# Kernel optimization log

Measured on AMD Instinct MI355X. Metric: run time of the kernel, lower is better.

Reference implementation:

```python
import jax, jax.numpy as jnp
import numpy as np

B, H, L, D = 2, 16, 1024, 64
LMAX = 2048  # max_sequence_length: patterns built & normalized at LMAX, then sliced to L
PI = float(np.pi)


def _scale_pattern(freq):
    # pattern[h, t, d] = exp(i(t+ph)) + exp(i(2t+ph)) + exp(i(0.5t+ph)), ph = 2*pi*h/H
    # identical across d, so keep [H, L, 1] and broadcast over D
    phase = 2.0 * PI * jnp.arange(H, dtype=jnp.float32) / H          # [H]
    t = jnp.linspace(0.0, 2.0 * PI * freq, LMAX)                     # [LMAX]
    a1 = t[None, :] + phase[:, None]
    a2 = 2.0 * t[None, :] + phase[:, None]
    a3 = 0.5 * t[None, :] + phase[:, None]
    pr = jnp.cos(a1) + jnp.cos(a2) + jnp.cos(a3)                     # [H, LMAX]
    pi_ = jnp.sin(a1) + jnp.sin(a2) + jnp.sin(a3)
    norm = jnp.sqrt(jnp.sum(pr * pr + pi_ * pi_, axis=1, keepdims=True))  # over full LMAX
    pr, pi_ = pr / norm, pi_ / norm
    return pr[:, :L, None], pi_[:, :L, None]                          # [H, L, 1]


def _expert_total_pattern():
    # 8 experts x 3 aspects; pattern[t, d] = exp(i(f*t + 2*pi*d/D)), normalized per
    # column over LMAX (|exp|=1 -> norm sqrt(LMAX)). Elementwise complex multiply is
    # linear, so the expert stage equals x * sum(all patterns)/(sqrt(3)*sqrt(8)).
    freqs = np.array([[0.3 + 0.1 * i, 0.2 + 0.1 * i, 0.1 + 0.1 * i]
                      for i in range(8)], dtype=np.float32).reshape(-1)   # [24]
    t = jnp.linspace(0.0, 2.0 * PI, LMAX)                                 # [LMAX]
    phase_d = 2.0 * PI * jnp.arange(D, dtype=jnp.float32) / D             # [D]
    ang = jnp.asarray(freqs)[:, None, None] * t[None, :, None] + phase_d[None, None, :]  # [24, LMAX, D]
    col_norm = 1.0 / np.sqrt(float(LMAX))
    denom = np.sqrt(3.0) * np.sqrt(8.0)
    pr = jnp.sum(jnp.cos(ang), axis=0) * (col_norm / denom)               # [LMAX, D]
    pi_ = jnp.sum(jnp.sin(ang), axis=0) * (col_norm / denom)
    return pr[:L], pi_[:L]                                                # [L, D]


def _process_scale(Qr, Qi, Kr, Ki, Vr, Vi, pr, pi_):
    # complex elementwise pattern multiply
    Qpr = Qr * pr - Qi * pi_
    Qpi = Qr * pi_ + Qi * pr
    Kpr = Kr * pr - Ki * pi_
    Kpi = Kr * pi_ + Ki * pr
    # complex scores = Qp @ Kp^T (no conjugation, matching the torch code)
    sr = jnp.einsum('bhld,bhmd->bhlm', Qpr, Kpr) - jnp.einsum('bhld,bhmd->bhlm', Qpi, Kpi)
    si = jnp.einsum('bhld,bhmd->bhlm', Qpr, Kpi) + jnp.einsum('bhld,bhmd->bhlm', Qpi, Kpr)
    mag = jnp.sqrt(sr * sr + si * si) / np.sqrt(float(D))
    w = jax.nn.softmax(mag, axis=-1)
    return (jnp.einsum('bhlm,bhmd->bhld', w, Vr),
            jnp.einsum('bhlm,bhmd->bhld', w, Vi))


def reference(Q_real, Q_imag, K_real, K_imag, V_real, V_imag):
    scale_freqs = [1.0, 0.5, 0.25, 0.1]  # char, word, phrase, sentence
    acc_r = jnp.zeros_like(Q_real)
    acc_i = jnp.zeros_like(Q_real)
    for f in scale_freqs:
        pr, pi_ = _scale_pattern(f)
        o_r, o_i = _process_scale(Q_real, Q_imag, K_real, K_imag, V_real, V_imag, pr, pi_)
        acc_r = acc_r + o_r
        acc_i = acc_i + o_i
    inv = 1.0 / np.sqrt(float(len(scale_freqs)))
    acc_r = acc_r * inv
    acc_i = acc_i * inv
    # expert mixing (linear in x -> single fused complex elementwise multiply)
    epr, epi = _expert_total_pattern()  # [L, D], broadcast over B,H
    out_r = acc_r * epr - acc_i * epi
    out_i = acc_r * epi + acc_i * epr
    return jnp.stack([out_r, out_i], axis=0)  # [2, B, H, L, D] (real, imag)


def setup_inputs() -> dict:
    key = jax.random.key(0)
    ks = jax.random.split(key, 6)
    shape = (B, H, L, D)
    names = ['Q_real', 'Q_imag', 'K_real', 'K_imag', 'V_real', 'V_imag']
    return {n: jax.random.normal(k, shape, dtype=jnp.float32) for n, k in zip(names, ks)}
```

## Files before the change

kernel.cpp:

```cpp
#include <hip/hip_runtime.h>
#include <math.h>

typedef short bf16x8 __attribute__((ext_vector_type(8)));
typedef float f32x4 __attribute__((ext_vector_type(4)));

#define BDIM 256
constexpr int B_ = 2, H_ = 16, L_ = 1024, D_ = 64, LMAX_ = 2048;
constexpr int BH_ = B_ * H_;
constexpr float PI_F = 3.14159265358979323846f;

constexpr int WS_SVP = 0;
constexpr int WS_KBR = 65536;
constexpr int WS_KBI = WS_KBR + 1048576;
constexpr int WS_VTR = WS_KBI + 1048576;
constexpr int WS_VTI = WS_VTR + 1048576;

__device__ __forceinline__ unsigned short f2b(float x) {
    union { float f; unsigned u; } v; v.f = x;
    return (unsigned short)((v.u + 0x8000u) >> 16);
}
__device__ __forceinline__ unsigned pk2(float a, float b) {
    union { float f; unsigned u; } va, vb; va.f = a; vb.f = b;
    return ((va.u + 0x8000u) >> 16) | ((vb.u + 0x8000u) & 0xFFFF0000u);
}
__device__ __forceinline__ uint4 pack4(const float4& a, const float4& b) {
    return make_uint4(pk2(a.x, a.y), pk2(a.z, a.w), pk2(b.x, b.y), pk2(b.z, b.w));
}

#define MFMA(a, b, c) __builtin_amdgcn_mfma_f32_16x16x32_bf16((a), (b), (c), 0, 0, 0)

__device__ __forceinline__ float a_val(int s, int l, float4 invn) {
    const float fr = (s == 0) ? 1.0f : (s == 1) ? 0.5f : (s == 2) ? 0.25f : 0.1f;
    const float iv = (s == 0) ? invn.x : (s == 1) ? invn.y : (s == 2) ? invn.z : invn.w;
    float t = (2.0f * PI_F * fr / (float)(LMAX_ - 1)) * (float)l;
    float m2 = 3.0f + 2.0f * cosf(t) + 2.0f * cosf(0.5f * t) + 2.0f * cosf(1.5f * t);
    return sqrtf(fmaxf(m2, 0.0f)) * iv;
}

__global__ __launch_bounds__(BDIM)
void prep_kernel(const float* __restrict__ Kr, const float* __restrict__ Ki,
                 const float* __restrict__ Vr, const float* __restrict__ Vi,
                 float* __restrict__ ws) {
    const int tid = threadIdx.x;
    const int blk = blockIdx.x;
    unsigned short* KbR = (unsigned short*)(ws + WS_KBR);
    unsigned short* KbI = (unsigned short*)(ws + WS_KBI);
    unsigned short* VtR = (unsigned short*)(ws + WS_VTR);
    unsigned short* VtI = (unsigned short*)(ws + WS_VTI);

    if (blk < 256) {
        const int comp = blk >> 7;
        const float* src = comp ? Ki : Kr;
        unsigned short* dst = comp ? KbI : KbR;
        size_t b0 = (size_t)(blk & 127) * 16384;
#pragma unroll
        for (int i = 0; i < 4; ++i) {
            size_t e = b0 + (size_t)(i * 256 + tid) * 16;
            float4 x0 = *(const float4*)(src + e);
            float4 x1 = *(const float4*)(src + e + 4);
            float4 x2 = *(const float4*)(src + e + 8);
            float4 x3 = *(const float4*)(src + e + 12);
            *(uint4*)(dst + e) = pack4(x0, x1);
            *(uint4*)(dst + e + 8) = pack4(x2, x3);
        }
    } else {
        __shared__ unsigned short sT[64 * 70];
        __shared__ float sRed[4 * 64];
        const int vb = blk - 256;
        const int comp = vb & 1, mt = (vb >> 1) & 15, bh = vb >> 5;
        const int m0 = mt * 64;
        const float* src = (comp ? Vi : Vr) + (size_t)bh * 65536 + (size_t)m0 * 64;
        unsigned short* dstA = (comp ? VtI : VtR) + (size_t)bh * 65536;
#pragma unroll
        for (int i = 0; i < 4; ++i) {
            int e = i * 256 + tid;
            int m = e >> 4, d4 = (e & 15) * 4;
            float4 x = *(const float4*)(src + (size_t)m * 64 + d4);
            *(uint2*)&sT[m * 70 + d4] = make_uint2(pk2(x.x, x.y), pk2(x.z, x.w));
        }
        {
            int d = tid & 63, grp = tid >> 6;
            float s = 0.0f;
#pragma unroll
            for (int k = 0; k < 16; ++k) s += src[(size_t)(grp * 16 + k) * 64 + d];
            sRed[grp * 64 + d] = s;
        }
        __syncthreads();
        {
            int d = tid >> 2, ms = (tid & 3) * 16;
            unsigned short v[16];
#pragma unroll
            for (int k = 0; k < 16; ++k) v[k] = sT[(ms + k) * 70 + d];
            unsigned short* dst = dstA + (size_t)d * 1024 + m0 + ms;
            *(uint4*)dst = make_uint4((unsigned)v[0] | ((unsigned)v[1] << 16),
                                      (unsigned)v[2] | ((unsigned)v[3] << 16),
                                      (unsigned)v[4] | ((unsigned)v[5] << 16),
                                      (unsigned)v[6] | ((unsigned)v[7] << 16));
            *(uint4*)(dst + 8) = make_uint4((unsigned)v[8] | ((unsigned)v[9] << 16),
                                            (unsigned)v[10] | ((unsigned)v[11] << 16),
                                            (unsigned)v[12] | ((unsigned)v[13] << 16),
                                            (unsigned)v[14] | ((unsigned)v[15] << 16));
        }
        if (tid < 64)
            ws[WS_SVP + comp * 32768 + bh * 1024 + mt * 64 + tid] =
                sRed[tid] + sRed[64 + tid] + sRed[128 + tid] + sRed[192 + tid];
    }
}

__device__ __forceinline__ void stage64s(const unsigned short* g0, int stride,
                                         unsigned short* lds, int w, int lane) {
#pragma unroll
    for (int i = 0; i < 2; ++i) {
        int c = w * 2 + i;
        int lrow = c * 8 + (lane >> 3);
        int lg = (lane & 7) ^ (lrow & 7);
        const unsigned short* src = g0 + (size_t)lrow * stride + lg * 8;
        __builtin_amdgcn_global_load_lds(
            (const __attribute__((address_space(1))) void*)src,
            (__attribute__((address_space(3))) void*)(lds + c * 512), 16, 0, 0);
    }
}
__device__ __forceinline__ bf16x8 ldfrag(const unsigned short* b, int row, int g) {
    return *(const bf16x8*)&b[row * 64 + ((g ^ (row & 7)) << 3)];
}

__global__ __launch_bounds__(BDIM, 2)
void attn_kernel(const float* __restrict__ Qr, const float* __restrict__ Qi,
                 const float* __restrict__ ws, float* __restrict__ out, float4 invn) {
    __shared__ unsigned short sK0[2][4096], sK1[2][4096];
    __shared__ unsigned short sV0[4096], sV1[4096];
    __shared__ unsigned short sE[4096];
    __shared__ unsigned short sMg[4096];
    __shared__ unsigned short sAmb[4 * 1032];
    __shared__ float sDen[4 * 64];

    const int tid = threadIdx.x;
    const int lane = tid & 63;
    const int w = tid >> 6;
    const int lo16 = lane & 15;
    const int quad = lane >> 4;
    const int blk = blockIdx.x;
    const int bh = (blk & 7) * 4 + (blk >> 7);
    const int qt = (blk >> 3) & 15;
    const int l0 = qt * 64;
    const size_t base = (size_t)bh * (L_ * D_);

    const unsigned short* gKr = (const unsigned short*)(ws + WS_KBR) + (size_t)bh * 65536;
    const unsigned short* gKi = (const unsigned short*)(ws + WS_KBI) + (size_t)bh * 65536;
    const unsigned short* gVr = (const unsigned short*)(ws + WS_VTR) + (size_t)bh * 65536;
    const unsigned short* gVi = (const unsigned short*)(ws + WS_VTI) + (size_t)bh * 65536;

    stage64s(gKr, 64, sK0[0], w, lane);
    stage64s(gKi, 64, sK1[0], w, lane);

    for (int e = tid; e < 4096; e += BDIM) {
        int s = e >> 10, l = e & 1023;
        sAmb[s * 1032 + l] = f2b(a_val(s, l, invn) * 0.125f);
    }

    bf16x8 fQr0, fQr1, fQi0, fQi1, fnQi0, fnQi1;
    {
        const int ql = l0 + w * 16 + lo16;
        const float* qr = Qr + base + (size_t)ql * 64;
        const float* qi = Qi + base + (size_t)ql * 64;
        float4 a0 = *(const float4*)(qr + quad * 8);
        float4 a1 = *(const float4*)(qr + quad * 8 + 4);
        float4 b0 = *(const float4*)(qr + 32 + quad * 8);
        float4 b1 = *(const float4*)(qr + 32 + quad * 8 + 4);
        *(uint4*)&fQr0 = pack4(a0, a1);
        *(uint4*)&fQr1 = pack4(b0, b1);
        a0 = *(const float4*)(qi + quad * 8);
        a1 = *(const float4*)(qi + quad * 8 + 4);
        b0 = *(const float4*)(qi + 32 + quad * 8);
        b1 = *(const float4*)(qi + 32 + quad * 8 + 4);
        *(uint4*)&fQi0 = pack4(a0, a1);
        *(uint4*)&fQi1 = pack4(b0, b1);
        uint4 t0 = *(uint4*)&fQi0, t1 = *(uint4*)&fQi1;
        t0.x ^= 0x80008000u; t0.y ^= 0x80008000u; t0.z ^= 0x80008000u; t0.w ^= 0x80008000u;
        t1.x ^= 0x80008000u; t1.y ^= 0x80008000u; t1.z ^= 0x80008000u; t1.w ^= 0x80008000u;
        *(uint4*)&fnQi0 = t0; *(uint4*)&fnQi1 = t1;
    }

    bf16x8 uf1a = (bf16x8){0, 0, 0, 0, 0, 0, 0, 0};
    uf1a[0] = (short)f2b(a_val(quad, l0 + w * 16 + lo16, invn) * (1.0f / 1024.0f));

    f32x4 accM1 = (f32x4){0.f, 0.f, 0.f, 0.f};
    f32x4 aOutR[4], aOutI[4];
#pragma unroll
    for (int dt = 0; dt < 4; ++dt) {
        aOutR[dt] = (f32x4){0.f, 0.f, 0.f, 0.f};
        aOutI[dt] = (f32x4){0.f, 0.f, 0.f, 0.f};
    }

    __syncthreads();

    int cur = 0;
#pragma unroll 1
    for (int mt = 0; mt < 16; ++mt) {
        const int m0 = mt * 64;
        stage64s(gVr + m0, 1024, sV0, w, lane);
        stage64s(gVi + m0, 1024, sV1, w, lane);
        if (mt < 15) {
            stage64s(gKr + (size_t)(m0 + 64) * 64, 64, sK0[cur ^ 1], w, lane);
            stage64s(gKi + (size_t)(m0 + 64) * 64, 64, sK1[cur ^ 1], w, lane);
        }
        const unsigned short* cK0 = sK0[cur];
        const unsigned short* cK1 = sK1[cur];

#pragma unroll
        for (int ct = 0; ct < 4; ++ct) {
            const int mrow = ct * 16 + lo16;
            bf16x8 kr0 = ldfrag(cK0, mrow, quad), kr1 = ldfrag(cK0, mrow, quad + 4);
            bf16x8 ki0 = ldfrag(cK1, mrow, quad), ki1 = ldfrag(cK1, mrow, quad + 4);
            f32x4 aR = (f32x4){0.f, 0.f, 0.f, 0.f};
            f32x4 aI = (f32x4){0.f, 0.f, 0.f, 0.f};
            __builtin_amdgcn_s_setprio(1);
            aR = MFMA(kr0, fQr0, aR);  aR = MFMA(kr1, fQr1, aR);
            aR = MFMA(ki0, fnQi0, aR); aR = MFMA(ki1, fnQi1, aR);
            aI = MFMA(ki0, fQr0, aI);  aI = MFMA(ki1, fQr1, aI);
            aI = MFMA(kr0, fQi0, aI);  aI = MFMA(kr1, fQi1, aI);
            __builtin_amdgcn_s_setprio(0);
            float mg0 = sqrtf(fmaf(aR[0], aR[0], aI[0] * aI[0]));
            float mg1 = sqrtf(fmaf(aR[1], aR[1], aI[1] * aI[1]));
            float mg2 = sqrtf(fmaf(aR[2], aR[2], aI[2] * aI[2]));
            float mg3 = sqrtf(fmaf(aR[3], aR[3], aI[3] * aI[3]));
            bf16x8 bf1 = (bf16x8){0, 0, 0, 0, 0, 0, 0, 0};
            bf1[0] = (short)sAmb[quad * 1032 + m0 + ct * 16 + lo16];
            f32x4 z = (f32x4){0.f, 0.f, 0.f, 0.f};
            f32x4 a1 = MFMA(bf1, uf1a, z);
            float p0 = mg0 * a1[0], p1 = mg1 * a1[1];
            float p2 = mg2 * a1[2], p3 = mg3 * a1[3];
            int l = w * 16 + lo16;
            int gph = (ct * 2 + (quad >> 1)) ^ (l & 7);
            *(uint2*)&sE[l * 64 + gph * 8 + (quad & 1) * 4] =
                make_uint2(pk2(p0, p1), pk2(p2, p3));
            *(uint2*)&sMg[l * 64 + gph * 8 + (quad & 1) * 4] =
                make_uint2(pk2(mg0, mg1), pk2(mg2, mg3));
        }
        {
            bf16x8 mf0 = ldfrag(sMg, w * 16 + lo16, quad);
            bf16x8 mf1 = ldfrag(sMg, w * 16 + lo16, quad + 4);
            bf16x8 b0 = (bf16x8){0, 0, 0, 0, 0, 0, 0, 0};
            bf16x8 b1 = (bf16x8){0, 0, 0, 0, 0, 0, 0, 0};
            if (lo16 < 4) {
                b0 = *(const bf16x8*)&sAmb[lo16 * 1032 + m0 + quad * 8];
                b1 = *(const bf16x8*)&sAmb[lo16 * 1032 + m0 + 32 + quad * 8];
            }
            accM1 = MFMA(mf0, b0, accM1);
            accM1 = MFMA(mf1, b1, accM1);
        }
        if (mt < 15) {
            asm volatile("s_waitcnt vmcnt(4)" ::: "memory");
        } else {
            asm volatile("s_waitcnt vmcnt(0)" ::: "memory");
        }
        __builtin_amdgcn_s_barrier();
        {
            bf16x8 pa0 = ldfrag(sE, w * 16 + lo16, quad);
            bf16x8 pa1 = ldfrag(sE, w * 16 + lo16, quad + 4);
            __builtin_amdgcn_s_setprio(1);
#pragma unroll
            for (int dt = 0; dt < 4; ++dt) {
                int dr = dt * 16 + lo16;
                bf16x8 vr0 = ldfrag(sV0, dr, quad), vr1 = ldfrag(sV0, dr, quad + 4);
                bf16x8 vi0 = ldfrag(sV1, dr, quad), vi1 = ldfrag(sV1, dr, quad + 4);
                aOutR[dt] = MFMA(pa0, vr0, aOutR[dt]);
                aOutR[dt] = MFMA(pa1, vr1, aOutR[dt]);
                aOutI[dt] = MFMA(pa0, vi0, aOutI[dt]);
                aOutI[dt] = MFMA(pa1, vi1, aOutI[dt]);
            }
            __builtin_amdgcn_s_setprio(0);
        }
        asm volatile("s_waitcnt vmcnt(0)" ::: "memory");
        __builtin_amdgcn_s_barrier();
        cur ^= 1;
    }

    if (lo16 < 4) {
#pragma unroll
        for (int reg = 0; reg < 4; ++reg) {
            int r = w * 16 + quad * 4 + reg;
            float alv = a_val(lo16, l0 + r, invn);
            sDen[lo16 * 64 + r] = 1.0f / (1024.0f + alv * accM1[reg]);
        }
    }
    float cden[4];
#pragma unroll
    for (int reg = 0; reg < 4; ++reg) {
        int r = w * 16 + quad * 4 + reg;
        cden[reg] = sDen[r] + sDen[64 + r] + sDen[128 + r] + sDen[192 + r];
    }

    const float cE = rsqrtf(2048.0f) * rsqrtf(24.0f);
    float eRr[4], eRi[4];
#pragma unroll
    for (int reg = 0; reg < 4; ++reg) {
        int lrow = l0 + w * 16 + quad * 4 + reg;
        float tl = (2.0f * PI_F / (float)(LMAX_ - 1)) * (float)lrow;
        float s1, c1;
        __sincosf(0.1f * tl, &s1, &c1);
        const float W[10] = {1.f, 2.f, 3.f, 3.f, 3.f, 3.f, 3.f, 3.f, 2.f, 1.f};
        float cr = c1, ci = s1;
        float er = W[0] * cr, ei = W[0] * ci;
#pragma unroll
        for (int k = 1; k < 10; ++k) {
            float nr = cr * c1 - ci * s1;
            float ni = cr * s1 + ci * c1;
            cr = nr; ci = ni;
            er = fmaf(W[k], cr, er);
            ei = fmaf(W[k], ci, ei);
        }
        eRr[reg] = er * cE;
        eRi[reg] = ei * cE;
    }

    const size_t ooff = (size_t)BH_ * L_ * D_;
#pragma unroll
    for (int dt = 0; dt < 4; ++dt) {
        int d = dt * 16 + lo16;
        float svr = 0.0f, svi = 0.0f;
#pragma unroll
        for (int q = 0; q < 16; ++q) {
            svr += ws[WS_SVP + bh * 1024 + q * 64 + d];
            svi += ws[WS_SVP + 32768 + bh * 1024 + q * 64 + d];
        }
        float sp, cp;
        __sincosf((2.0f * PI_F / 64.0f) * (float)d, &sp, &cp);
#pragma unroll
        for (int reg = 0; reg < 4; ++reg) {
            int lrow = l0 + w * 16 + quad * 4 + reg;
            float numR = fmaf(cden[reg], svr, aOutR[dt][reg]) * 0.5f;
            float numI = fmaf(cden[reg], svi, aOutI[dt][reg]) * 0.5f;
            float epr = cp * eRr[reg] - sp * eRi[reg];
            float epi = sp * eRr[reg] + cp * eRi[reg];
            size_t o = base + (size_t)lrow * 64 + d;
            out[o] = numR * epr - numI * epi;
            out[o + ooff] = numR * epi + numI * epr;
        }
    }
}

extern "C" void kernel_launch(void* const* d_in, const int* in_sizes, int n_in,
                              void* d_out, int out_size, void* d_ws, size_t ws_size,
                              hipStream_t stream) {
    const float* Qr = (const float*)d_in[0];
    const float* Qi = (const float*)d_in[1];
    const float* Kr = (const float*)d_in[2];
    const float* Ki = (const float*)d_in[3];
    const float* Vr = (const float*)d_in[4];
    const float* Vi = (const float*)d_in[5];
    float* ws = (float*)d_ws;
    float* out = (float*)d_out;

    const double fr[4] = {1.0, 0.5, 0.25, 0.1};
    float inv[4];
    for (int s = 0; s < 4; ++s) {
        double a = 2.0 * 3.14159265358979323846 * fr[s] / (double)(LMAX_ - 1);
        double S = 3.0 * LMAX_;
        const double mul[3] = {1.0, 0.5, 1.5};
        for (int k = 0; k < 3; ++k) {
            double x = a * mul[k];
            S += 2.0 * (cos(x * 1023.5) * sin(x * 1024.0) / sin(x * 0.5));
        }
        inv[s] = (float)(1.0 / sqrt(S));
    }
    float4 invn = make_float4(inv[0], inv[1], inv[2], inv[3]);

    prep_kernel<<<1280, BDIM, 0, stream>>>(Kr, Ki, Vr, Vi, ws);
    attn_kernel<<<512, BDIM, 0, stream>>>(Qr, Qi, ws, out, invn);
}
```

Baseline: 152.2 us.

## Fuse prep and attention into one cooperative kernel with grid sync

Merges the K/V bf16 conversion and transpose prep kernel into the attention kernel, using a cooperative launch and a grid-wide sync between the two phases. Shared memory is a union so the prep scratch reuses the attention buffers. The per-row amplitude values are now read back from the LDS table instead of being recomputed with cosines. This removes one kernel launch and its gap, at the cost of a grid barrier and a fallback to two kernels if the cooperative launch fails.

New measurement: 287.7 us. 89.1% more time.

```diff
diff --git a/kernel.cpp b/kernel.cpp
--- a/kernel.cpp
+++ b/kernel.cpp
@@ -1,5 +1,8 @@
 #include <hip/hip_runtime.h>
+#include <hip/hip_cooperative_groups.h>
 #include <math.h>
+
+namespace cg = cooperative_groups;
 
 typedef short bf16x8 __attribute__((ext_vector_type(8)));
 typedef float f32x4 __attribute__((ext_vector_type(4)));
@@ -18,6 +21,10 @@
 __device__ __forceinline__ unsigned short f2b(float x) {
     union { float f; unsigned u; } v; v.f = x;
     return (unsigned short)((v.u + 0x8000u) >> 16);
+}
+__device__ __forceinline__ float b2f(unsigned short x) {
+    union { unsigned u; float f; } v; v.u = ((unsigned)x) << 16;
+    return v.f;
 }
 __device__ __forceinline__ unsigned pk2(float a, float b) {
     union { float f; unsigned u; } va, vb; va.f = a; vb.f = b;
@@ -37,75 +44,19 @@
     return sqrtf(fmaxf(m2, 0.0f)) * iv;
 }
 
-__global__ __launch_bounds__(BDIM)
-void prep_kernel(const float* __restrict__ Kr, const float* __restrict__ Ki,
-                 const float* __restrict__ Vr, const float* __restrict__ Vi,
-                 float* __restrict__ ws) {
-    const int tid = threadIdx.x;
-    const int blk = blockIdx.x;
-    unsigned short* KbR = (unsigned short*)(ws + WS_KBR);
-    unsigned short* KbI = (unsigned short*)(ws + WS_KBI);
-    unsigned short* VtR = (unsigned short*)(ws + WS_VTR);
-    unsigned short* VtI = (unsigned short*)(ws + WS_VTI);
-
-    if (blk < 256) {
-        const int comp = blk >> 7;
-        const float* src = comp ? Ki : Kr;
-        unsigned short* dst = comp ? KbI : KbR;
-        size_t b0 = (size_t)(blk & 127) * 16384;
-#pragma unroll
-        for (int i = 0; i < 4; ++i) {
-            size_t e = b0 + (size_t)(i * 256 + tid) * 16;
-            float4 x0 = *(const float4*)(src + e);
-            float4 x1 = *(const float4*)(src + e + 4);
-            float4 x2 = *(const float4*)(src + e + 8);
-            float4 x3 = *(const float4*)(src + e + 12);
-            *(uint4*)(dst + e) = pack4(x0, x1);
-            *(uint4*)(dst + e + 8) = pack4(x2, x3);
-        }
-    } else {
-        __shared__ unsigned short sT[64 * 70];
-        __shared__ float sRed[4 * 64];
-        const int vb = blk - 256;
-        const int comp = vb & 1, mt = (vb >> 1) & 15, bh = vb >> 5;
-        const int m0 = mt * 64;
-        const float* src = (comp ? Vi : Vr) + (size_t)bh * 65536 + (size_t)m0 * 64;
-        unsigned short* dstA = (comp ? VtI : VtR) + (size_t)bh * 65536;
-#pragma unroll
-        for (int i = 0; i < 4; ++i) {
-            int e = i * 256 + tid;
-            int m = e >> 4, d4 = (e & 15) * 4;
-            float4 x = *(const float4*)(src + (size_t)m * 64 + d4);
-            *(uint2*)&sT[m * 70 + d4] = make_uint2(pk2(x.x, x.y), pk2(x.z, x.w));
-        }
-        {
-            int d = tid & 63, grp = tid >> 6;
-            float s = 0.0f;
-#pragma unroll
-            for (int k = 0; k < 16; ++k) s += src[(size_t)(grp * 16 + k) * 64 + d];
-            sRed[grp * 64 + d] = s;
-        }
-        __syncthreads();
-        {
-            int d = tid >> 2, ms = (tid & 3) * 16;
-            unsigned short v[16];
-#pragma unroll
-            for (int k = 0; k < 16; ++k) v[k] = sT[(ms + k) * 70 + d];
-            unsigned short* dst = dstA + (size_t)d * 1024 + m0 + ms;
-            *(uint4*)dst = make_uint4((unsigned)v[0] | ((unsigned)v[1] << 16),
-                                      (unsigned)v[2] | ((unsigned)v[3] << 16),
-                                      (unsigned)v[4] | ((unsigned)v[5] << 16),
-                                      (unsigned)v[6] | ((unsigned)v[7] << 16));
-            *(uint4*)(dst + 8) = make_uint4((unsigned)v[8] | ((unsigned)v[9] << 16),
-                                            (unsigned)v[10] | ((unsigned)v[11] << 16),
-                                            (unsigned)v[12] | ((unsigned)v[13] << 16),
-                                            (unsigned)v[14] | ((unsigned)v[15] << 16));
-        }
-        if (tid < 64)
-            ws[WS_SVP + comp * 32768 + bh * 1024 + mt * 64 + tid] =
-                sRed[tid] + sRed[64 + tid] + sRed[128 + tid] + sRed[192 + tid];
-    }
-}
+union SMem {
+    struct {
+        unsigned short sK0[2][4096], sK1[2][4096];
+        unsigned short sV0[4096], sV1[4096];
+        unsigned short sE[4096], sMg[4096];
+        unsigned short sAmb[4 * 1032];
+        float sDen[4 * 64];
+    } a;
+    struct {
+        unsigned short sT[64 * 70];
+        float sRed[4 * 64];
+    } p;
+};
 
 __device__ __forceinline__ void stage64s(const unsigned short* g0, int stride,
                                          unsigned short* lds, int w, int lane) {
@@ -124,16 +75,59 @@
     return *(const bf16x8*)&b[row * 64 + ((g ^ (row & 7)) << 3)];
 }
 
-__global__ __launch_bounds__(BDIM, 2)
-void attn_kernel(const float* __restrict__ Qr, const float* __restrict__ Qi,
-                 const float* __restrict__ ws, float* __restrict__ out, float4 invn) {
-    __shared__ unsigned short sK0[2][4096], sK1[2][4096];
-    __shared__ unsigned short sV0[4096], sV1[4096];
-    __shared__ unsigned short sE[4096];
-    __shared__ unsigned short sMg[4096];
-    __shared__ unsigned short sAmb[4 * 1032];
-    __shared__ float sDen[4 * 64];
-
+__device__ __forceinline__ void vt_tile(int vb, const float* __restrict__ Vr,
+                                        const float* __restrict__ Vi,
+                                        float* __restrict__ ws, SMem& sm) {
+    const int tid = threadIdx.x;
+    const int comp = vb & 1, mt = (vb >> 1) & 15, bh = vb >> 5;
+    const int m0 = mt * 64;
+    unsigned short* VtR = (unsigned short*)(ws + WS_VTR);
+    unsigned short* VtI = (unsigned short*)(ws + WS_VTI);
+    const float* src = (comp ? Vi : Vr) + (size_t)bh * 65536 + (size_t)m0 * 64;
+    unsigned short* dstA = (comp ? VtI : VtR) + (size_t)bh * 65536;
+    __syncthreads();
+#pragma unroll
+    for (int i = 0; i < 4; ++i) {
+        int e = i * 256 + tid;
+        int m = e >> 4, d4 = (e & 15) * 4;
+        float4 x = *(const float4*)(src + (size_t)m * 64 + d4);
+        *(uint2*)&sm.p.sT[m * 70 + d4] = make_uint2(pk2(x.x, x.y), pk2(x.z, x.w));
+    }
+    {
+        int d = tid & 63, grp = tid >> 6;
+        float s = 0.0f;
+#pragma unroll
+        for (int k = 0; k < 16; ++k) s += src[(size_t)(grp * 16 + k) * 64 + d];
+        sm.p.sRed[grp * 64 + d] = s;
+    }
+    __syncthreads();
+    {
+        int d = tid >> 2, ms = (tid & 3) * 16;
+        unsigned short v[16];
+#pragma unroll
+        for (int k = 0; k < 16; ++k) v[k] = sm.p.sT[(ms + k) * 70 + d];
+        unsigned short* dst = dstA + (size_t)d * 1024 + m0 + ms;
+        *(uint4*)dst = make_uint4((unsigned)v[0] | ((unsigned)v[1] << 16),
+                                  (unsigned)v[2] | ((unsigned)v[3] << 16),
+                                  (unsigned)v[4] | ((unsigned)v[5] << 16),
+                                  (unsigned)v[6] | ((unsigned)v[7] << 16));
+        *(uint4*)(dst + 8) = make_uint4((unsigned)v[8] | ((unsigned)v[9] << 16),
+                                        (unsigned)v[10] | ((unsigned)v[11] << 16),
+                                        (unsigned)v[12] | ((unsigned)v[13] << 16),
+                                        (unsigned)v[14] | ((unsigned)v[15] << 16));
+    }
+    if (tid < 64)
+        ws[WS_SVP + comp * 32768 + bh * 1024 + mt * 64 + tid] =
+            sm.p.sRed[tid] + sm.p.sRed[64 + tid] + sm.p.sRed[128 + tid] +
+            sm.p.sRed[192 + tid];
+}
+
+__device__ __forceinline__ void attn_body(const float* __restrict__ Qr,
+                                          const float* __restrict__ Qi,
+                                          const float* __restrict__ ws,
+                                          float* __restrict__ out, float4 invn,
+                                          SMem& sm, bool fillAmb) {
+    auto& A = sm.a;
     const int tid = threadIdx.x;
     const int lane = tid & 63;
     const int w = tid >> 6;
@@ -150,12 +144,14 @@
     const unsigned short* gVr = (const unsigned short*)(ws + WS_VTR) + (size_t)bh * 65536;
     const unsigned short* gVi = (const unsigned short*)(ws + WS_VTI) + (size_t)bh * 65536;
 
-    stage64s(gKr, 64, sK0[0], w, lane);
-    stage64s(gKi, 64, sK1[0], w, lane);
-
-    for (int e = tid; e < 4096; e += BDIM) {
-        int s = e >> 10, l = e & 1023;
-        sAmb[s * 1032 + l] = f2b(a_val(s, l, invn) * 0.125f);
+    stage64s(gKr, 64, A.sK0[0], w, lane);
+    stage64s(gKi, 64, A.sK1[0], w, lane);
+
+    if (fillAmb) {
+        for (int e = tid; e < 4096; e += BDIM) {
+            int s = e >> 10, l = e & 1023;
+            A.sAmb[s * 1032 + l] = f2b(a_val(s, l, invn) * 0.125f);
+        }
     }
 
     bf16x8 fQr0, fQr1, fQi0, fQi1, fnQi0, fnQi1;
@@ -181,9 +177,6 @@
         *(uint4*)&fnQi0 = t0; *(uint4*)&fnQi1 = t1;
     }
 
-    bf16x8 uf1a = (bf16x8){0, 0, 0, 0, 0, 0, 0, 0};
-    uf1a[0] = (short)f2b(a_val(quad, l0 + w * 16 + lo16, invn) * (1.0f / 1024.0f));
-
     f32x4 accM1 = (f32x4){0.f, 0.f, 0.f, 0.f};
     f32x4 aOutR[4], aOutI[4];
 #pragma unroll
@@ -193,19 +186,23 @@
     }
 
     __syncthreads();
+
+    bf16x8 uf1a = (bf16x8){0, 0, 0, 0, 0, 0, 0, 0};
+    uf1a[0] = (short)f2b(b2f(A.sAmb[quad * 1032 + (l0 + w * 16 + lo16)]) *
+                         (1.0f / 128.0f));
 
     int cur = 0;
 #pragma unroll 1
     for (int mt = 0; mt < 16; ++mt) {
         const int m0 = mt * 64;
-        stage64s(gVr + m0, 1024, sV0, w, lane);
-        stage64s(gVi + m0, 1024, sV1, w, lane);
+        stage64s(gVr + m0, 1024, A.sV0, w, lane);
+        stage64s(gVi + m0, 1024, A.sV1, w, lane);
         if (mt < 15) {
-            stage64s(gKr + (size_t)(m0 + 64) * 64, 64, sK0[cur ^ 1], w, lane);
-            stage64s(gKi + (size_t)(m0 + 64) * 64, 64, sK1[cur ^ 1], w, lane);
-        }
-        const unsigned short* cK0 = sK0[cur];
-        const unsigned short* cK1 = sK1[cur];
+            stage64s(gKr + (size_t)(m0 + 64) * 64, 64, A.sK0[cur ^ 1], w, lane);
+            stage64s(gKi + (size_t)(m0 + 64) * 64, 64, A.sK1[cur ^ 1], w, lane);
+        }
+        const unsigned short* cK0 = A.sK0[cur];
+        const unsigned short* cK1 = A.sK1[cur];
 
 #pragma unroll
         for (int ct = 0; ct < 4; ++ct) {
@@ -225,26 +222,26 @@
             float mg2 = sqrtf(fmaf(aR[2], aR[2], aI[2] * aI[2]));
             float mg3 = sqrtf(fmaf(aR[3], aR[3], aI[3] * aI[3]));
             bf16x8 bf1 = (bf16x8){0, 0, 0, 0, 0, 0, 0, 0};
-            bf1[0] = (short)sAmb[quad * 1032 + m0 + ct * 16 + lo16];
+            bf1[0] = (short)A.sAmb[quad * 1032 + m0 + ct * 16 + lo16];
             f32x4 z = (f32x4){0.f, 0.f, 0.f, 0.f};
             f32x4 a1 = MFMA(bf1, uf1a, z);
             float p0 = mg0 * a1[0], p1 = mg1 * a1[1];
             float p2 = mg2 * a1[2], p3 = mg3 * a1[3];
             int l = w * 16 + lo16;
             int gph = (ct * 2 + (quad >> 1)) ^ (l & 7);
-            *(uint2*)&sE[l * 64 + gph * 8 + (quad & 1) * 4] =
+            *(uint2*)&A.sE[l * 64 + gph * 8 + (quad & 1) * 4] =
                 make_uint2(pk2(p0, p1), pk2(p2, p3));
-            *(uint2*)&sMg[l * 64 + gph * 8 + (quad & 1) * 4] =
+            *(uint2*)&A.sMg[l * 64 + gph * 8 + (quad & 1) * 4] =
                 make_uint2(pk2(mg0, mg1), pk2(mg2, mg3));
         }
         {
-            bf16x8 mf0 = ldfrag(sMg, w * 16 + lo16, quad);
-            bf16x8 mf1 = ldfrag(sMg, w * 16 + lo16, quad + 4);
+            bf16x8 mf0 = ldfrag(A.sMg, w * 16 + lo16, quad);
+            bf16x8 mf1 = ldfrag(A.sMg, w * 16 + lo16, quad + 4);
             bf16x8 b0 = (bf16x8){0, 0, 0, 0, 0, 0, 0, 0};
             bf16x8 b1 = (bf16x8){0, 0, 0, 0, 0, 0, 0, 0};
             if (lo16 < 4) {
-                b0 = *(const bf16x8*)&sAmb[lo16 * 1032 + m0 + quad * 8];
-                b1 = *(const bf16x8*)&sAmb[lo16 * 1032 + m0 + 32 + quad * 8];
+                b0 = *(const bf16x8*)&A.sAmb[lo16 * 1032 + m0 + quad * 8];
+                b1 = *(const bf16x8*)&A.sAmb[lo16 * 1032 + m0 + 32 + quad * 8];
             }
             accM1 = MFMA(mf0, b0, accM1);
             accM1 = MFMA(mf1, b1, accM1);
@@ -256,14 +253,14 @@
         }
         __builtin_amdgcn_s_barrier();
         {
-            bf16x8 pa0 = ldfrag(sE, w * 16 + lo16, quad);
-            bf16x8 pa1 = ldfrag(sE, w * 16 + lo16, quad + 4);
+            bf16x8 pa0 = ldfrag(A.sE, w * 16 + lo16, quad);
+            bf16x8 pa1 = ldfrag(A.sE, w * 16 + lo16, quad + 4);
             __builtin_amdgcn_s_setprio(1);
 #pragma unroll
             for (int dt = 0; dt < 4; ++dt) {
                 int dr = dt * 16 + lo16;
-                bf16x8 vr0 = ldfrag(sV0, dr, quad), vr1 = ldfrag(sV0, dr, quad + 4);
-                bf16x8 vi0 = ldfrag(sV1, dr, quad), vi1 = ldfrag(sV1, dr, quad + 4);
+                bf16x8 vr0 = ldfrag(A.sV0, dr, quad), vr1 = ldfrag(A.sV0, dr, quad + 4);
+                bf16x8 vi0 = ldfrag(A.sV1, dr, quad), vi1 = ldfrag(A.sV1, dr, quad + 4);
                 aOutR[dt] = MFMA(pa0, vr0, aOutR[dt]);
                 aOutR[dt] = MFMA(pa1, vr1, aOutR[dt]);
                 aOutI[dt] = MFMA(pa0, vi0, aOutI[dt]);
@@ -280,15 +277,15 @@
 #pragma unroll
         for (int reg = 0; reg < 4; ++reg) {
             int r = w * 16 + quad * 4 + reg;
-            float alv = a_val(lo16, l0 + r, invn);
-            sDen[lo16 * 64 + r] = 1.0f / (1024.0f + alv * accM1[reg]);
+            float alv = b2f(A.sAmb[lo16 * 1032 + (l0 + r)]) * 8.0f;
+            A.sDen[lo16 * 64 + r] = 1.0f / (1024.0f + alv * accM1[reg]);
         }
     }
     float cden[4];
 #pragma unroll
     for (int reg = 0; reg < 4; ++reg) {
         int r = w * 16 + quad * 4 + reg;
-        cden[reg] = sDen[r] + sDen[64 + r] + sDen[128 + r] + sDen[192 + r];
+        cden[reg] = A.sDen[r] + A.sDen[64 + r] + A.sDen[128 + r] + A.sDen[192 + r];
     }
 
     const float cE = rsqrtf(2048.0f) * rsqrtf(24.0f);
@@ -338,6 +335,82 @@
             out[o + ooff] = numR * epi + numI * epr;
         }
     }
+}
+
+__global__ __launch_bounds__(BDIM, 2)
+void fused_kernel(const float* __restrict__ Qr, const float* __restrict__ Qi,
+                  const float* __restrict__ Kr, const float* __restrict__ Ki,
+                  const float* __restrict__ Vr, const float* __restrict__ Vi,
+                  float* __restrict__ ws, float* __restrict__ out, float4 invn) {
+    __shared__ SMem sm;
+    const int tid = threadIdx.x;
+    const int blk = blockIdx.x;
+
+    {
+        unsigned short* KbR = (unsigned short*)(ws + WS_KBR);
+        unsigned short* KbI = (unsigned short*)(ws + WS_KBI);
+        const int comp = blk >> 8;
+        const float* src = comp ? Ki : Kr;
+        unsigned short* dst = comp ? KbI : KbR;
+        size_t b0 = (size_t)(blk & 255) * 8192;
+#pragma unroll
+        for (int i = 0; i < 2; ++i) {
+            size_t e = b0 + (size_t)(i * 256 + tid) * 16;
+            float4 x0 = *(const float4*)(src + e);
+            float4 x1 = *(const float4*)(src + e + 4);
+            float4 x2 = *(const float4*)(src + e + 8);
+            float4 x3 = *(const float4*)(src + e + 12);
+            *(uint4*)(dst + e) = pack4(x0, x1);
+            *(uint4*)(dst + e + 8) = pack4(x2, x3);
+        }
+    }
+    for (int e = tid; e < 4096; e += BDIM) {
+        int s = e >> 10, l = e & 1023;
+        sm.a.sAmb[s * 1032 + l] = f2b(a_val(s, l, invn) * 0.125f);
+    }
+    vt_tile(blk * 2, Vr, Vi, ws, sm);
+    vt_tile(blk * 2 + 1, Vr, Vi, ws, sm);
+
+    __threadfence();
+    cg::this_grid().sync();
+
+    attn_body(Qr, Qi, ws, out, invn, sm, false);
+}
+
+__global__ __launch_bounds__(BDIM)
+void prep_kernel(const float* __restrict__ Kr, const float* __restrict__ Ki,
+                 const float* __restrict__ Vr, const float* __restrict__ Vi,
+                 float* __restrict__ ws) {
+    __shared__ SMem sm;
+    const int tid = threadIdx.x;
+    const int blk = blockIdx.x;
+    if (blk < 256) {
+        unsigned short* KbR = (unsigned short*)(ws + WS_KBR);
+        unsigned short* KbI = (unsigned short*)(ws + WS_KBI);
+        const int comp = blk >> 7;
+        const float* src = comp ? Ki : Kr;
+        unsigned short* dst = comp ? KbI : KbR;
+        size_t b0 = (size_t)(blk & 127) * 16384;
+#pragma unroll
+        for (int i = 0; i < 4; ++i) {
+            size_t e = b0 + (size_t)(i * 256 + tid) * 16;
+            float4 x0 = *(const float4*)(src + e);
+            float4 x1 = *(const float4*)(src + e + 4);
+            float4 x2 = *(const float4*)(src + e + 8);
+            float4 x3 = *(const float4*)(src + e + 12);
+            *(uint4*)(dst + e) = pack4(x0, x1);
+            *(uint4*)(dst + e + 8) = pack4(x2, x3);
+        }
+    } else {
+        vt_tile(blk - 256, Vr, Vi, ws, sm);
+    }
+}
+
+__global__ __launch_bounds__(BDIM, 2)
+void attn_kernel(const float* __restrict__ Qr, const float* __restrict__ Qi,
+                 const float* __restrict__ ws, float* __restrict__ out, float4 invn) {
+    __shared__ SMem sm;
+    attn_body(Qr, Qi, ws, out, invn, sm, true);
 }
 
 extern "C" void kernel_launch(void* const* d_in, const int* in_sizes, int n_in,
@@ -366,6 +439,12 @@
     }
     float4 invn = make_float4(inv[0], inv[1], inv[2], inv[3]);
 
-    prep_kernel<<<1280, BDIM, 0, stream>>>(Kr, Ki, Vr, Vi, ws);
-    attn_kernel<<<512, BDIM, 0, stream>>>(Qr, Qi, ws, out, invn);
-}
+    void* args[] = {(void*)&Qr, (void*)&Qi, (void*)&Kr, (void*)&Ki,
+                    (void*)&Vr, (void*)&Vi, (void*)&ws, (void*)&out, (void*)&invn};
+    hipError_t err = hipLaunchCooperativeKernel(fused_kernel, dim3(512), dim3(BDIM),
+                                                args, 0, stream);
+    if (err != hipSuccess) {
+        prep_kernel<<<1280, BDIM, 0, stream>>>(Kr, Ki, Vr, Vi, ws);
+        attn_kernel<<<512, BDIM, 0, stream>>>(Qr, Qi, ws, out, invn);
+    }
+}
```

## Double-buffer V tiles, compute magnitude sums in registers, transpose SVP layout

Applied to the files above, without the earlier changes.

V tiles are now double-buffered alongside K and prefetched one iteration ahead, so each loop iteration needs one barrier instead of two. The per-row magnitude-weighted sums are accumulated in registers with FMAs and cross-lane shuffles, replacing the sMg LDS round trip and the extra MFMAs. The partial-sum workspace is stored transposed so the epilogue can read it with contiguous float4 loads. These changes cost more LDS for the second V buffer and extra per-lane FMA work, and the LDS padding on sAmb is dropped, which may bring back bank conflicts.

Result: slower. 155.4 us (+2.1%).

```diff
diff --git a/kernel.cpp b/kernel.cpp
--- a/kernel.cpp
+++ b/kernel.cpp
@@ -18,6 +18,18 @@
 __device__ __forceinline__ unsigned short f2b(float x) {
     union { float f; unsigned u; } v; v.f = x;
     return (unsigned short)((v.u + 0x8000u) >> 16);
+}
+__device__ __forceinline__ float b2f(unsigned short x) {
+    union { unsigned u; float f; } v; v.u = ((unsigned)x) << 16;
+    return v.f;
+}
+__device__ __forceinline__ float blo(unsigned u) {
+    union { unsigned u; float f; } v; v.u = u << 16;
+    return v.f;
+}
+__device__ __forceinline__ float bhi(unsigned u) {
+    union { unsigned u; float f; } v; v.u = u & 0xFFFF0000u;
+    return v.f;
 }
 __device__ __forceinline__ unsigned pk2(float a, float b) {
     union { float f; unsigned u; } va, vb; va.f = a; vb.f = b;
@@ -102,7 +114,7 @@
                                             (unsigned)v[14] | ((unsigned)v[15] << 16));
         }
         if (tid < 64)
-            ws[WS_SVP + comp * 32768 + bh * 1024 + mt * 64 + tid] =
+            ws[WS_SVP + comp * 32768 + bh * 1024 + tid * 16 + mt] =
                 sRed[tid] + sRed[64 + tid] + sRed[128 + tid] + sRed[192 + tid];
     }
 }
@@ -128,11 +140,9 @@
 void attn_kernel(const float* __restrict__ Qr, const float* __restrict__ Qi,
                  const float* __restrict__ ws, float* __restrict__ out, float4 invn) {
     __shared__ unsigned short sK0[2][4096], sK1[2][4096];
-    __shared__ unsigned short sV0[4096], sV1[4096];
+    __shared__ unsigned short sV0[2][4096], sV1[2][4096];
     __shared__ unsigned short sE[4096];
-    __shared__ unsigned short sMg[4096];
-    __shared__ unsigned short sAmb[4 * 1032];
-    __shared__ float sDen[4 * 64];
+    __shared__ unsigned short sAmb[4 * 1024];
 
     const int tid = threadIdx.x;
     const int lane = tid & 63;
@@ -152,10 +162,12 @@
 
     stage64s(gKr, 64, sK0[0], w, lane);
     stage64s(gKi, 64, sK1[0], w, lane);
+    stage64s(gVr, 1024, sV0[0], w, lane);
+    stage64s(gVi, 1024, sV1[0], w, lane);
 
     for (int e = tid; e < 4096; e += BDIM) {
         int s = e >> 10, l = e & 1023;
-        sAmb[s * 1032 + l] = f2b(a_val(s, l, invn) * 0.125f);
+        sAmb[s * 1024 + l] = f2b(a_val(s, l, invn) * 0.125f);
     }
 
     bf16x8 fQr0, fQr1, fQi0, fQi1, fnQi0, fnQi1;
@@ -181,10 +193,13 @@
         *(uint4*)&fnQi0 = t0; *(uint4*)&fnQi1 = t1;
     }
 
+    __syncthreads();
+
     bf16x8 uf1a = (bf16x8){0, 0, 0, 0, 0, 0, 0, 0};
-    uf1a[0] = (short)f2b(a_val(quad, l0 + w * 16 + lo16, invn) * (1.0f / 1024.0f));
-
-    f32x4 accM1 = (f32x4){0.f, 0.f, 0.f, 0.f};
+    uf1a[0] = (short)f2b(b2f(sAmb[quad * 1024 + (l0 + w * 16 + lo16)]) *
+                         (1.0f / 128.0f));
+
+    float macc[4] = {0.f, 0.f, 0.f, 0.f};
     f32x4 aOutR[4], aOutI[4];
 #pragma unroll
     for (int dt = 0; dt < 4; ++dt) {
@@ -192,17 +207,17 @@
         aOutI[dt] = (f32x4){0.f, 0.f, 0.f, 0.f};
     }
 
-    __syncthreads();
-
-    int cur = 0;
 #pragma unroll 1
     for (int mt = 0; mt < 16; ++mt) {
         const int m0 = mt * 64;
-        stage64s(gVr + m0, 1024, sV0, w, lane);
-        stage64s(gVi + m0, 1024, sV1, w, lane);
+        const int cur = mt & 1;
+        asm volatile("s_waitcnt vmcnt(0)" ::: "memory");
+        __builtin_amdgcn_s_barrier();
         if (mt < 15) {
             stage64s(gKr + (size_t)(m0 + 64) * 64, 64, sK0[cur ^ 1], w, lane);
             stage64s(gKi + (size_t)(m0 + 64) * 64, 64, sK1[cur ^ 1], w, lane);
+            stage64s(gVr + m0 + 64, 1024, sV0[cur ^ 1], w, lane);
+            stage64s(gVi + m0 + 64, 1024, sV1[cur ^ 1], w, lane);
         }
         const unsigned short* cK0 = sK0[cur];
         const unsigned short* cK1 = sK1[cur];
@@ -224,8 +239,16 @@
             float mg1 = sqrtf(fmaf(aR[1], aR[1], aI[1] * aI[1]));
             float mg2 = sqrtf(fmaf(aR[2], aR[2], aI[2] * aI[2]));
             float mg3 = sqrtf(fmaf(aR[3], aR[3], aI[3] * aI[3]));
+#pragma unroll
+            for (int s = 0; s < 4; ++s) {
+                uint2 av = *(const uint2*)&sAmb[s * 1024 + m0 + ct * 16 + quad * 4];
+                macc[s] = fmaf(mg0, blo(av.x),
+                          fmaf(mg1, bhi(av.x),
+                          fmaf(mg2, blo(av.y),
+                          fmaf(mg3, bhi(av.y), macc[s]))));
+            }
             bf16x8 bf1 = (bf16x8){0, 0, 0, 0, 0, 0, 0, 0};
-            bf1[0] = (short)sAmb[quad * 1032 + m0 + ct * 16 + lo16];
+            bf1[0] = (short)sAmb[quad * 1024 + m0 + ct * 16 + lo16];
             f32x4 z = (f32x4){0.f, 0.f, 0.f, 0.f};
             f32x4 a1 = MFMA(bf1, uf1a, z);
             float p0 = mg0 * a1[0], p1 = mg1 * a1[1];
@@ -234,27 +257,7 @@
             int gph = (ct * 2 + (quad >> 1)) ^ (l & 7);
             *(uint2*)&sE[l * 64 + gph * 8 + (quad & 1) * 4] =
                 make_uint2(pk2(p0, p1), pk2(p2, p3));
-            *(uint2*)&sMg[l * 64 + gph * 8 + (quad & 1) * 4] =
-                make_uint2(pk2(mg0, mg1), pk2(mg2, mg3));
-        }
-        {
-            bf16x8 mf0 = ldfrag(sMg, w * 16 + lo16, quad);
-            bf16x8 mf1 = ldfrag(sMg, w * 16 + lo16, quad + 4);
-            bf16x8 b0 = (bf16x8){0, 0, 0, 0, 0, 0, 0, 0};
-            bf16x8 b1 = (bf16x8){0, 0, 0, 0, 0, 0, 0, 0};
-            if (lo16 < 4) {
-                b0 = *(const bf16x8*)&sAmb[lo16 * 1032 + m0 + quad * 8];
-                b1 = *(const bf16x8*)&sAmb[lo16 * 1032 + m0 + 32 + quad * 8];
-            }
-            accM1 = MFMA(mf0, b0, accM1);
-            accM1 = MFMA(mf1, b1, accM1);
-        }
-        if (mt < 15) {
-            asm volatile("s_waitcnt vmcnt(4)" ::: "memory");
-        } else {
-            asm volatile("s_waitcnt vmcnt(0)" ::: "memory");
-        }
-        __builtin_amdgcn_s_barrier();
+        }
         {
             bf16x8 pa0 = ldfrag(sE, w * 16 + lo16, quad);
             bf16x8 pa1 = ldfrag(sE, w * 16 + lo16, quad + 4);
@@ -262,8 +265,8 @@
 #pragma unroll
             for (int dt = 0; dt < 4; ++dt) {
                 int dr = dt * 16 + lo16;
-                bf16x8 vr0 = ldfrag(sV0, dr, quad), vr1 = ldfrag(sV0, dr, quad + 4);
-                bf16x8 vi0 = ldfrag(sV1, dr, quad), vi1 = ldfrag(sV1, dr, quad + 4);
+                bf16x8 vr0 = ldfrag(sV0[cur], dr, quad), vr1 = ldfrag(sV0[cur], dr, quad + 4);
+                bf16x8 vi0 = ldfrag(sV1[cur], dr, quad), vi1 = ldfrag(sV1[cur], dr, quad + 4);
                 aOutR[dt] = MFMA(pa0, vr0, aOutR[dt]);
                 aOutR[dt] = MFMA(pa1, vr1, aOutR[dt]);
                 aOutI[dt] = MFMA(pa0, vi0, aOutI[dt]);
@@ -271,25 +274,23 @@
             }
             __builtin_amdgcn_s_setprio(0);
         }
-        asm volatile("s_waitcnt vmcnt(0)" ::: "memory");
-        __builtin_amdgcn_s_barrier();
-        cur ^= 1;
-    }
-
-    if (lo16 < 4) {
-#pragma unroll
-        for (int reg = 0; reg < 4; ++reg) {
-            int r = w * 16 + quad * 4 + reg;
-            float alv = a_val(lo16, l0 + r, invn);
-            sDen[lo16 * 64 + r] = 1.0f / (1024.0f + alv * accM1[reg]);
-        }
-    }
-    float cden[4];
-#pragma unroll
-    for (int reg = 0; reg < 4; ++reg) {
-        int r = w * 16 + quad * 4 + reg;
-        cden[reg] = sDen[r] + sDen[64 + r] + sDen[128 + r] + sDen[192 + r];
-    }
+    }
+
+#pragma unroll
+    for (int s = 0; s < 4; ++s) {
+        macc[s] += __shfl_xor(macc[s], 16);
+        macc[s] += __shfl_xor(macc[s], 32);
+    }
+    float cden = 0.0f;
+#pragma unroll
+    for (int s = 0; s < 4; ++s) {
+        float alv = b2f(sAmb[s * 1024 + (l0 + w * 16 + lo16)]) * 8.0f;
+        cden += 1.0f / (1024.0f + alv * macc[s]);
+    }
+    float cdenR[4];
+#pragma unroll
+    for (int reg = 0; reg < 4; ++reg)
+        cdenR[reg] = __shfl(cden, quad * 4 + reg);
 
     const float cE = rsqrtf(2048.0f) * rsqrtf(24.0f);
     float eRr[4], eRi[4];
@@ -318,19 +319,27 @@
 #pragma unroll
     for (int dt = 0; dt < 4; ++dt) {
         int d = dt * 16 + lo16;
-        float svr = 0.0f, svi = 0.0f;
-#pragma unroll
-        for (int q = 0; q < 16; ++q) {
-            svr += ws[WS_SVP + bh * 1024 + q * 64 + d];
-            svi += ws[WS_SVP + 32768 + bh * 1024 + q * 64 + d];
-        }
+        const float* svp = ws + WS_SVP + bh * 1024 + (size_t)d * 16;
+        float4 r0 = *(const float4*)(svp);
+        float4 r1 = *(const float4*)(svp + 4);
+        float4 r2 = *(const float4*)(svp + 8);
+        float4 r3 = *(const float4*)(svp + 12);
+        float svr = (r0.x + r0.y + r0.z + r0.w) + (r1.x + r1.y + r1.z + r1.w) +
+                    (r2.x + r2.y + r2.z + r2.w) + (r3.x + r3.y + r3.z + r3.w);
+        const float* svq = svp + 32768;
+        r0 = *(const float4*)(svq);
+        r1 = *(const float4*)(svq + 4);
+        r2 = *(const float4*)(svq + 8);
+        r3 = *(const float4*)(svq + 12);
+        float svi = (r0.x + r0.y + r0.z + r0.w) + (r1.x + r1.y + r1.z + r1.w) +
+                    (r2.x + r2.y + r2.z + r2.w) + (r3.x + r3.y + r3.z + r3.w);
         float sp, cp;
         __sincosf((2.0f * PI_F / 64.0f) * (float)d, &sp, &cp);
 #pragma unroll
         for (int reg = 0; reg < 4; ++reg) {
             int lrow = l0 + w * 16 + quad * 4 + reg;
-            float numR = fmaf(cden[reg], svr, aOutR[dt][reg]) * 0.5f;
-            float numI = fmaf(cden[reg], svi, aOutI[dt][reg]) * 0.5f;
+            float numR = fmaf(cdenR[reg], svr, aOutR[dt][reg]) * 0.5f;
+            float numI = fmaf(cdenR[reg], svi, aOutI[dt][reg]) * 0.5f;
             float epr = cp * eRr[reg] - sp * eRi[reg];
             float epi = sp * eRr[reg] + cp * eRi[reg];
             size_t o = base + (size_t)lrow * 64 + d;
```
